# Kernel optimization log

Measured on AMD Instinct MI355X. Metric: run time of the kernel, lower is better.

The kernel has to match this reference:

```python
import jax, jax.numpy as jnp
import numpy as np

B, T, D_IN, H = 4096, 256, 128, 64


def setup_inputs() -> dict:
    key = jax.random.key(0)
    ks = jax.random.split(key, 12)
    s_in = 1.0 / np.sqrt(H)  # torch GRU init scale (uniform +-1/sqrt(hidden))
    u = lambda k, shape: jax.random.uniform(k, shape, jnp.float32, -s_in, s_in)
    return {
        "x": jax.random.normal(ks[0], (B, T, D_IN), jnp.float32),
        "W_ih0": u(ks[1], (3 * H, D_IN)),
        "W_hh0": u(ks[2], (3 * H, H)),
        "b_ih0": u(ks[3], (3 * H,)),
        "b_hh0": u(ks[4], (3 * H,)),
        "W_ih1": u(ks[5], (3 * H, H)),
        "W_hh1": u(ks[6], (3 * H, H)),
        "b_ih1": u(ks[7], (3 * H,)),
        "b_hh1": u(ks[8], (3 * H,)),
        "W_fc": u(ks[9], (1, H)),
        "b_fc": u(ks[10], (1,)),
    }


def _gru_layer(x_seq, W_ih, W_hh, b_ih, b_hh):
    # x_seq: [B, T, D]; returns (all hidden states [B, T, H], last hidden [B, H])
    # Precompute input projections for all timesteps (one big GEMM).
    gx = jnp.einsum("btd,gd->btg", x_seq, W_ih) + b_ih  # [B, T, 3H]
    gx = jnp.swapaxes(gx, 0, 1)  # [T, B, 3H] for scan
    h0 = jnp.zeros((x_seq.shape[0], H), x_seq.dtype)

    def step(h, gx_t):
        gh = h @ W_hh.T + b_hh  # [B, 3H]
        # PyTorch gate order: r, z, n
        gx_r, gx_z, gx_n = jnp.split(gx_t, 3, axis=-1)
        gh_r, gh_z, gh_n = jnp.split(gh, 3, axis=-1)
        r = jax.nn.sigmoid(gx_r + gh_r)
        z = jax.nn.sigmoid(gx_z + gh_z)
        n = jnp.tanh(gx_n + r * gh_n)
        h_new = (1.0 - z) * n + z * h
        return h_new, h_new

    h_last, hs = jax.lax.scan(step, h0, gx)
    return jnp.swapaxes(hs, 0, 1), h_last


def reference(x, W_ih0, W_hh0, b_ih0, b_hh0, W_ih1, W_hh1, b_ih1, b_hh1, W_fc, b_fc):
    h1_seq, _ = _gru_layer(x, W_ih0, W_hh0, b_ih0, b_hh0)
    _, h2_last = _gru_layer(h1_seq, W_ih1, W_hh1, b_ih1, b_hh1)
    return h2_last @ W_fc.T + b_fc  # [B, 1]
```

## Files before the change

kernel.cpp:

```cpp
#include <hip/hip_runtime.h>


#define TT  256
#define DIN 128
#define HH  64

typedef _Float16 f16x8 __attribute__((ext_vector_type(8)));
typedef float    f32x4 __attribute__((ext_vector_type(4)));

__device__ __forceinline__ float fast_sigmoid(float x) {
    float e = __builtin_amdgcn_exp2f(-1.44269504088896f * x);
    return __builtin_amdgcn_rcpf(1.0f + e);
}
__device__ __forceinline__ float fast_tanh(float x) {
    float e = __builtin_amdgcn_exp2f(2.88539008177793f * x);
    return 1.0f - 2.0f * __builtin_amdgcn_rcpf(1.0f + e);
}

__device__ __forceinline__ void lds_barrier() {
    asm volatile("s_waitcnt lgkmcnt(0)" ::: "memory");
    __builtin_amdgcn_s_barrier();
    asm volatile("" ::: "memory");
}

__global__ __launch_bounds__(256, 1) void gru_fused_kernel(
    const float* __restrict__ x,
    const float* __restrict__ Wih0, const float* __restrict__ Whh0,
    const float* __restrict__ bih0, const float* __restrict__ bhh0,
    const float* __restrict__ Wih1, const float* __restrict__ Whh1,
    const float* __restrict__ bih1, const float* __restrict__ bhh1,
    const float* __restrict__ Wfc,  const float* __restrict__ bfc,
    float* __restrict__ out)
{
    const int tid  = threadIdx.x;
    const int wv   = tid >> 6;
    const int lane = tid & 63;
    const int q    = lane >> 4;
    const int lm   = lane & 15;
    const int cw   = wv << 4;
    const int b0   = blockIdx.x << 4;

    __shared__ __align__(16) _Float16 h1buf[2][16][HH + 8];
    __shared__ __align__(16) _Float16 h2buf[2][16][HH + 8];
    __shared__ float ored[4][16];

    const float* xrow = x + (size_t)(b0 + lm) * TT * DIN + q * 8;
    float4 xa0[8], xa1[8];
    auto prefetch = [&](int t, float4 (&xb)[8]) {
        const float* p = xrow + t * DIN;
        #pragma unroll
        for (int s = 0; s < 4; s++) {
            xb[2 * s]     = *(const float4*)(p + s * 32);
            xb[2 * s + 1] = *(const float4*)(p + s * 32 + 4);
        }
    };
    prefetch(0, xa0);
    prefetch(1, xa1);

    f16x8 wih0[3][4], whh0[3][2], wih1[3][2], whh1[3][2];
    float bi0[3], bh0[3], bi1[3], bh1[3];
    #pragma unroll
    for (int g = 0; g < 3; g++) {
        const int n = g * 64 + cw + lm;
        #pragma unroll
        for (int s = 0; s < 4; s++) {
            const float* p = Wih0 + n * DIN + s * 32 + q * 8;
            #pragma unroll
            for (int j = 0; j < 8; j++) wih0[g][s][j] = (_Float16)p[j];
        }
        #pragma unroll
        for (int s = 0; s < 2; s++) {
            const float* ph = Whh0 + n * HH + s * 32 + q * 8;
            const float* pi = Wih1 + n * HH + s * 32 + q * 8;
            const float* pj = Whh1 + n * HH + s * 32 + q * 8;
            #pragma unroll
            for (int j = 0; j < 8; j++) {
                whh0[g][s][j] = (_Float16)ph[j];
                wih1[g][s][j] = (_Float16)pi[j];
                whh1[g][s][j] = (_Float16)pj[j];
            }
        }
        bi0[g] = bih0[n]; bh0[g] = bhh0[n];
        bi1[g] = bih1[n]; bh1[g] = bhh1[n];
    }

    {
        _Float16* z1 = &h1buf[0][0][0];
        _Float16* z2 = &h2buf[0][0][0];
        const int total = 2 * 16 * (HH + 8);
        for (int i = tid; i < total; i += 256) { z1[i] = (_Float16)0; z2[i] = (_Float16)0; }
    }
    float h1C[4] = {0.f, 0.f, 0.f, 0.f};
    float h2C[4] = {0.f, 0.f, 0.f, 0.f};
    __syncthreads();

    auto step = [&](int t, float4 (&xb)[8]) {
        const int p = t & 1;

        f16x8 ax[4];
        #pragma unroll
        for (int s = 0; s < 4; s++) {
            const float4 u = xb[2 * s], v = xb[2 * s + 1];
            ax[s][0] = (_Float16)u.x; ax[s][1] = (_Float16)u.y;
            ax[s][2] = (_Float16)u.z; ax[s][3] = (_Float16)u.w;
            ax[s][4] = (_Float16)v.x; ax[s][5] = (_Float16)v.y;
            ax[s][6] = (_Float16)v.z; ax[s][7] = (_Float16)v.w;
        }
        if (t + 2 < TT) prefetch(t + 2, xb);

        f16x8 ah1[2];
        ah1[0] = *(const f16x8*)&h1buf[p][lm][q * 8];
        ah1[1] = *(const f16x8*)&h1buf[p][lm][32 + q * 8];

        f32x4 agx[3], agh[3];
        #pragma unroll
        for (int g = 0; g < 3; g++) agx[g] = (f32x4){bi0[g], bi0[g], bi0[g], bi0[g]};
        #pragma unroll
        for (int s = 0; s < 4; s++)
            #pragma unroll
            for (int g = 0; g < 3; g++)
                agx[g] = __builtin_amdgcn_mfma_f32_16x16x32_f16(ax[s], wih0[g][s], agx[g], 0, 0, 0);
        #pragma unroll
        for (int g = 0; g < 3; g++) agh[g] = (f32x4){bh0[g], bh0[g], bh0[g], bh0[g]};
        #pragma unroll
        for (int s = 0; s < 2; s++)
            #pragma unroll
            for (int g = 0; g < 3; g++)
                agh[g] = __builtin_amdgcn_mfma_f32_16x16x32_f16(ah1[s], whh0[g][s], agh[g], 0, 0, 0);

        #pragma unroll
        for (int r = 0; r < 4; r++) {
            const float rr = fast_sigmoid(agx[0][r] + agh[0][r]);
            const float zz = fast_sigmoid(agx[1][r] + agh[1][r]);
            const float nn = fast_tanh(agx[2][r] + rr * agh[2][r]);
            h1C[r] = nn + zz * (h1C[r] - nn);
            h1buf[1 - p][q * 4 + r][cw + lm] = (_Float16)h1C[r];
        }
        lds_barrier();

        f16x8 ah1n[2], ah2[2];
        ah1n[0] = *(const f16x8*)&h1buf[1 - p][lm][q * 8];
        ah1n[1] = *(const f16x8*)&h1buf[1 - p][lm][32 + q * 8];
        ah2[0]  = *(const f16x8*)&h2buf[p][lm][q * 8];
        ah2[1]  = *(const f16x8*)&h2buf[p][lm][32 + q * 8];

        #pragma unroll
        for (int g = 0; g < 3; g++) {
            agx[g] = (f32x4){bi1[g], bi1[g], bi1[g], bi1[g]};
            agh[g] = (f32x4){bh1[g], bh1[g], bh1[g], bh1[g]};
        }
        #pragma unroll
        for (int s = 0; s < 2; s++)
            #pragma unroll
            for (int g = 0; g < 3; g++) {
                agx[g] = __builtin_amdgcn_mfma_f32_16x16x32_f16(ah1n[s], wih1[g][s], agx[g], 0, 0, 0);
                agh[g] = __builtin_amdgcn_mfma_f32_16x16x32_f16(ah2[s],  whh1[g][s], agh[g], 0, 0, 0);
            }
        #pragma unroll
        for (int r = 0; r < 4; r++) {
            const float rr = fast_sigmoid(agx[0][r] + agh[0][r]);
            const float zz = fast_sigmoid(agx[1][r] + agh[1][r]);
            const float nn = fast_tanh(agx[2][r] + rr * agh[2][r]);
            h2C[r] = nn + zz * (h2C[r] - nn);
            h2buf[1 - p][q * 4 + r][cw + lm] = (_Float16)h2C[r];
        }
    };

    for (int t = 0; t < TT; t += 2) {
        step(t, xa0);
        step(t + 1, xa1);
    }

    const float wf = Wfc[cw + lm];
    float pr[4];
    #pragma unroll
    for (int r = 0; r < 4; r++) pr[r] = h2C[r] * wf;
    #pragma unroll
    for (int m = 1; m < 16; m <<= 1) {
        #pragma unroll
        for (int r = 0; r < 4; r++) pr[r] += __shfl_xor(pr[r], m, 64);
    }
    if (lm == 0) {
        #pragma unroll
        for (int r = 0; r < 4; r++) ored[wv][q * 4 + r] = pr[r];
    }
    __syncthreads();
    if (tid < 16) {
        out[b0 + tid] = ored[0][tid] + ored[1][tid] + ored[2][tid] + ored[3][tid] + bfc[0];
    }
}

extern "C" void kernel_launch(void* const* d_in, const int* in_sizes, int n_in,
                              void* d_out, int out_size, void* d_ws, size_t ws_size,
                              hipStream_t stream) {
    (void)in_sizes; (void)n_in; (void)d_ws; (void)ws_size; (void)out_size;
    const float* x    = (const float*)d_in[0];
    const float* Wih0 = (const float*)d_in[1];
    const float* Whh0 = (const float*)d_in[2];
    const float* bih0 = (const float*)d_in[3];
    const float* bhh0 = (const float*)d_in[4];
    const float* Wih1 = (const float*)d_in[5];
    const float* Whh1 = (const float*)d_in[6];
    const float* bih1 = (const float*)d_in[7];
    const float* bhh1 = (const float*)d_in[8];
    const float* Wfc  = (const float*)d_in[9];
    const float* bfc  = (const float*)d_in[10];
    float* out = (float*)d_out;

    gru_fused_kernel<<<dim3(4096 / 16), dim3(256), 0, stream>>>(
        x, Wih0, Whh0, bih0, bhh0, Wih1, Whh1, bih1, bhh1, Wfc, bfc, out);
}
```

Baseline: 971.4 us.

## Split GRU layers across separate wave groups and pipeline them across timesteps

The block grows to 512 threads: waves 0-3 run layer 0 and waves 4-7 run layer 1, with layer 1 lagging one timestep behind. Each wave now keeps only one layer's weights in registers, and the two layers' dependency chains can overlap instead of running back to back within a step. This costs two barriers per step across eight waves and, with launch bounds of 512 threads and 2 blocks, a tighter register budget per thread.

```diff
diff --git a/kernel.cpp b/kernel.cpp
--- a/kernel.cpp
+++ b/kernel.cpp
@@ -23,7 +23,7 @@
     asm volatile("" ::: "memory");
 }
 
-__global__ __launch_bounds__(256, 1) void gru_fused_kernel(
+__global__ __launch_bounds__(512, 2) void gru_fused_kernel(
     const float* __restrict__ x,
     const float* __restrict__ Wih0, const float* __restrict__ Whh0,
     const float* __restrict__ bih0, const float* __restrict__ bhh0,
@@ -37,7 +37,8 @@
     const int lane = tid & 63;
     const int q    = lane >> 4;
     const int lm   = lane & 15;
-    const int cw   = wv << 4;
+    const bool isL0 = (wv < 4);
+    const int cw   = (wv & 3) << 4;
     const int b0   = blockIdx.x << 4;
 
     __shared__ __align__(16) _Float16 h1buf[2][16][HH + 8];
@@ -54,49 +55,53 @@
             xb[2 * s + 1] = *(const float4*)(p + s * 32 + 4);
         }
     };
-    prefetch(0, xa0);
-    prefetch(1, xa1);
-
-    f16x8 wih0[3][4], whh0[3][2], wih1[3][2], whh1[3][2];
-    float bi0[3], bh0[3], bi1[3], bh1[3];
+    if (isL0) { prefetch(0, xa0); prefetch(1, xa1); }
+
+    f16x8 wA[3][4], wB[3][2];
+    float bx[3], bh[3];
     #pragma unroll
     for (int g = 0; g < 3; g++) {
         const int n = g * 64 + cw + lm;
-        #pragma unroll
-        for (int s = 0; s < 4; s++) {
-            const float* p = Wih0 + n * DIN + s * 32 + q * 8;
-            #pragma unroll
-            for (int j = 0; j < 8; j++) wih0[g][s][j] = (_Float16)p[j];
-        }
-        #pragma unroll
-        for (int s = 0; s < 2; s++) {
-            const float* ph = Whh0 + n * HH + s * 32 + q * 8;
-            const float* pi = Wih1 + n * HH + s * 32 + q * 8;
-            const float* pj = Whh1 + n * HH + s * 32 + q * 8;
-            #pragma unroll
-            for (int j = 0; j < 8; j++) {
-                whh0[g][s][j] = (_Float16)ph[j];
-                wih1[g][s][j] = (_Float16)pi[j];
-                whh1[g][s][j] = (_Float16)pj[j];
-            }
-        }
-        bi0[g] = bih0[n]; bh0[g] = bhh0[n];
-        bi1[g] = bih1[n]; bh1[g] = bhh1[n];
+        if (isL0) {
+            #pragma unroll
+            for (int s = 0; s < 4; s++) {
+                const float* p = Wih0 + n * DIN + s * 32 + q * 8;
+                #pragma unroll
+                for (int j = 0; j < 8; j++) wA[g][s][j] = (_Float16)p[j];
+            }
+            #pragma unroll
+            for (int s = 0; s < 2; s++) {
+                const float* p = Whh0 + n * HH + s * 32 + q * 8;
+                #pragma unroll
+                for (int j = 0; j < 8; j++) wB[g][s][j] = (_Float16)p[j];
+            }
+            bx[g] = bih0[n]; bh[g] = bhh0[n];
+        } else {
+            #pragma unroll
+            for (int s = 0; s < 2; s++) {
+                const float* pa = Wih1 + n * HH + s * 32 + q * 8;
+                const float* pb = Whh1 + n * HH + s * 32 + q * 8;
+                #pragma unroll
+                for (int j = 0; j < 8; j++) {
+                    wA[g][s][j] = (_Float16)pa[j];
+                    wB[g][s][j] = (_Float16)pb[j];
+                }
+            }
+            bx[g] = bih1[n]; bh[g] = bhh1[n];
+        }
     }
 
     {
         _Float16* z1 = &h1buf[0][0][0];
         _Float16* z2 = &h2buf[0][0][0];
         const int total = 2 * 16 * (HH + 8);
-        for (int i = tid; i < total; i += 256) { z1[i] = (_Float16)0; z2[i] = (_Float16)0; }
-    }
-    float h1C[4] = {0.f, 0.f, 0.f, 0.f};
-    float h2C[4] = {0.f, 0.f, 0.f, 0.f};
+        for (int i = tid; i < total; i += 512) { z1[i] = (_Float16)0; z2[i] = (_Float16)0; }
+    }
+    float hC[4] = {0.f, 0.f, 0.f, 0.f};
     __syncthreads();
 
-    auto step = [&](int t, float4 (&xb)[8]) {
+    auto L0step = [&](int t, float4 (&xb)[8]) {
         const int p = t & 1;
-
         f16x8 ax[4];
         #pragma unroll
         for (int s = 0; s < 4; s++) {
@@ -108,81 +113,91 @@
         }
         if (t + 2 < TT) prefetch(t + 2, xb);
 
-        f16x8 ah1[2];
-        ah1[0] = *(const f16x8*)&h1buf[p][lm][q * 8];
-        ah1[1] = *(const f16x8*)&h1buf[p][lm][32 + q * 8];
+        f16x8 ah[2];
+        ah[0] = *(const f16x8*)&h1buf[p][lm][q * 8];
+        ah[1] = *(const f16x8*)&h1buf[p][lm][32 + q * 8];
 
         f32x4 agx[3], agh[3];
         #pragma unroll
-        for (int g = 0; g < 3; g++) agx[g] = (f32x4){bi0[g], bi0[g], bi0[g], bi0[g]};
+        for (int g = 0; g < 3; g++) agx[g] = (f32x4){bx[g], bx[g], bx[g], bx[g]};
         #pragma unroll
         for (int s = 0; s < 4; s++)
             #pragma unroll
             for (int g = 0; g < 3; g++)
-                agx[g] = __builtin_amdgcn_mfma_f32_16x16x32_f16(ax[s], wih0[g][s], agx[g], 0, 0, 0);
-        #pragma unroll
-        for (int g = 0; g < 3; g++) agh[g] = (f32x4){bh0[g], bh0[g], bh0[g], bh0[g]};
+                agx[g] = __builtin_amdgcn_mfma_f32_16x16x32_f16(ax[s], wA[g][s], agx[g], 0, 0, 0);
+        #pragma unroll
+        for (int g = 0; g < 3; g++) agh[g] = (f32x4){bh[g], bh[g], bh[g], bh[g]};
         #pragma unroll
         for (int s = 0; s < 2; s++)
             #pragma unroll
             for (int g = 0; g < 3; g++)
-                agh[g] = __builtin_amdgcn_mfma_f32_16x16x32_f16(ah1[s], whh0[g][s], agh[g], 0, 0, 0);
+                agh[g] = __builtin_amdgcn_mfma_f32_16x16x32_f16(ah[s], wB[g][s], agh[g], 0, 0, 0);
 
         #pragma unroll
         for (int r = 0; r < 4; r++) {
             const float rr = fast_sigmoid(agx[0][r] + agh[0][r]);
             const float zz = fast_sigmoid(agx[1][r] + agh[1][r]);
             const float nn = fast_tanh(agx[2][r] + rr * agh[2][r]);
-            h1C[r] = nn + zz * (h1C[r] - nn);
-            h1buf[1 - p][q * 4 + r][cw + lm] = (_Float16)h1C[r];
-        }
-        lds_barrier();
-
-        f16x8 ah1n[2], ah2[2];
-        ah1n[0] = *(const f16x8*)&h1buf[1 - p][lm][q * 8];
-        ah1n[1] = *(const f16x8*)&h1buf[1 - p][lm][32 + q * 8];
-        ah2[0]  = *(const f16x8*)&h2buf[p][lm][q * 8];
-        ah2[1]  = *(const f16x8*)&h2buf[p][lm][32 + q * 8];
-
+            hC[r] = nn + zz * (hC[r] - nn);
+            h1buf[1 - p][q * 4 + r][cw + lm] = (_Float16)hC[r];
+        }
+    };
+
+    auto L1step = [&](int t) {
+        const int w = (t + 1) & 1;
+        f16x8 ahx[2], ahh[2];
+        ahx[0] = *(const f16x8*)&h1buf[w][lm][q * 8];
+        ahx[1] = *(const f16x8*)&h1buf[w][lm][32 + q * 8];
+        ahh[0] = *(const f16x8*)&h2buf[1 - w][lm][q * 8];
+        ahh[1] = *(const f16x8*)&h2buf[1 - w][lm][32 + q * 8];
+
+        f32x4 agx[3], agh[3];
         #pragma unroll
         for (int g = 0; g < 3; g++) {
-            agx[g] = (f32x4){bi1[g], bi1[g], bi1[g], bi1[g]};
-            agh[g] = (f32x4){bh1[g], bh1[g], bh1[g], bh1[g]};
+            agx[g] = (f32x4){bx[g], bx[g], bx[g], bx[g]};
+            agh[g] = (f32x4){bh[g], bh[g], bh[g], bh[g]};
         }
         #pragma unroll
         for (int s = 0; s < 2; s++)
             #pragma unroll
             for (int g = 0; g < 3; g++) {
-                agx[g] = __builtin_amdgcn_mfma_f32_16x16x32_f16(ah1n[s], wih1[g][s], agx[g], 0, 0, 0);
-                agh[g] = __builtin_amdgcn_mfma_f32_16x16x32_f16(ah2[s],  whh1[g][s], agh[g], 0, 0, 0);
+                agx[g] = __builtin_amdgcn_mfma_f32_16x16x32_f16(ahx[s], wA[g][s], agx[g], 0, 0, 0);
+                agh[g] = __builtin_amdgcn_mfma_f32_16x16x32_f16(ahh[s], wB[g][s], agh[g], 0, 0, 0);
             }
         #pragma unroll
         for (int r = 0; r < 4; r++) {
             const float rr = fast_sigmoid(agx[0][r] + agh[0][r]);
             const float zz = fast_sigmoid(agx[1][r] + agh[1][r]);
             const float nn = fast_tanh(agx[2][r] + rr * agh[2][r]);
-            h2C[r] = nn + zz * (h2C[r] - nn);
-            h2buf[1 - p][q * 4 + r][cw + lm] = (_Float16)h2C[r];
+            hC[r] = nn + zz * (hC[r] - nn);
+            h2buf[w][q * 4 + r][cw + lm] = (_Float16)hC[r];
         }
     };
 
-    for (int t = 0; t < TT; t += 2) {
-        step(t, xa0);
-        step(t + 1, xa1);
-    }
-
-    const float wf = Wfc[cw + lm];
-    float pr[4];
-    #pragma unroll
-    for (int r = 0; r < 4; r++) pr[r] = h2C[r] * wf;
-    #pragma unroll
-    for (int m = 1; m < 16; m <<= 1) {
-        #pragma unroll
-        for (int r = 0; r < 4; r++) pr[r] += __shfl_xor(pr[r], m, 64);
-    }
-    if (lm == 0) {
-        #pragma unroll
-        for (int r = 0; r < 4; r++) ored[wv][q * 4 + r] = pr[r];
+    for (int k = 0; k < TT; k += 2) {
+        if (isL0)       L0step(k, xa0);
+        else if (k > 0) L1step(k - 1);
+        lds_barrier();
+        if (isL0) L0step(k + 1, xa1);
+        else      L1step(k);
+        lds_barrier();
+    }
+    if (!isL0) L1step(TT - 1);
+
+    if (!isL0) {
+        const float wf = Wfc[cw + lm];
+        float pr[4];
+        #pragma unroll
+        for (int r = 0; r < 4; r++) pr[r] = hC[r] * wf;
+        #pragma unroll
+        for (int m = 1; m < 16; m <<= 1) {
+            #pragma unroll
+            for (int r = 0; r < 4; r++) pr[r] += __shfl_xor(pr[r], m, 64);
+        }
+        if (lm == 0) {
+            #pragma unroll
+            for (int r = 0; r < 4; r++) ored[wv - 4][q * 4 + r] = pr[r];
+        }
     }
     __syncthreads();
     if (tid < 16) {
@@ -207,6 +222,6 @@
     const float* bfc  = (const float*)d_in[10];
     float* out = (float*)d_out;
 
-    gru_fused_kernel<<<dim3(4096 / 16), dim3(256), 0, stream>>>(
+    gru_fused_kernel<<<dim3(4096 / 16), dim3(512), 0, stream>>>(
         x, Wih0, Whh0, bih0, bhh0, Wih1, Whh1, bih1, bhh1, Wfc, bfc, out);
 }
```

Result: slower. 998.5 us (+2.8%).
